# Kernel optimization log

Measured on AMD Instinct MI355X. Metric: run time of the kernel, lower is better.

Reference implementation:

```python
import jax, jax.numpy as jnp
import numpy as np

L = 2          # num_hidden_layers
B, S, H = 2, 2048, 1024
NH, DH = 16, 64   # heads, head dim
FF = 4096
EPS = 1e-5


def setup_inputs() -> dict:
    key = jax.random.key(0)
    ks = jax.random.split(key, 20)
    s = 0.02
    inp = {
        "hidden_states": jax.random.normal(ks[0], (B, S, H), jnp.float32),
        "attention_mask": jnp.zeros((B, 1, 1, S), jnp.float32),
        "Wq": jax.random.normal(ks[1], (L, H, H), jnp.float32) * s,
        "bq": jnp.zeros((L, H), jnp.float32),
        "Wk": jax.random.normal(ks[2], (L, H, H), jnp.float32) * s,
        "bk": jnp.zeros((L, H), jnp.float32),
        "Wv": jax.random.normal(ks[3], (L, H, H), jnp.float32) * s,
        "bv": jnp.zeros((L, H), jnp.float32),
        "Wao": jax.random.normal(ks[4], (L, H, H), jnp.float32) * s,
        "bao": jnp.zeros((L, H), jnp.float32),
        "ln1_g": jnp.ones((L, H), jnp.float32),
        "ln1_b": jnp.zeros((L, H), jnp.float32),
        "Wi": jax.random.normal(ks[5], (L, H, FF), jnp.float32) * s,
        "bi": jnp.zeros((L, FF), jnp.float32),
        "Wo": jax.random.normal(ks[6], (L, FF, H), jnp.float32) * s,
        "bo": jnp.zeros((L, H), jnp.float32),
        "ln2_g": jnp.ones((L, H), jnp.float32),
        "ln2_b": jnp.zeros((L, H), jnp.float32),
    }
    return inp


def _layernorm(x, g, b):
    m = jnp.mean(x, axis=-1, keepdims=True)
    v = jnp.var(x, axis=-1, keepdims=True)
    return (x - m) * jax.lax.rsqrt(v + EPS) * g + b


def _split_heads(x):
    # [B,S,H] -> [B,NH,S,DH]
    return x.reshape(B, S, NH, DH).transpose(0, 2, 1, 3)


def _layer(x, mask, Wq, bq, Wk, bk, Wv, bv, Wao, bao, g1, b1, Wi, bi, Wo, bo, g2, b2):
    q = _split_heads(x @ Wq + bq)
    k = _split_heads(x @ Wk + bk)
    v = _split_heads(x @ Wv + bv)
    scores = jnp.einsum('bhqd,bhkd->bhqk', q, k) / np.sqrt(DH).astype(np.float32)
    scores = scores + mask  # additive attention mask
    probs = jax.nn.softmax(scores, axis=-1)
    ctx = jnp.einsum('bhqk,bhkd->bhqd', probs, v)
    ctx = ctx.transpose(0, 2, 1, 3).reshape(B, S, H)
    x = _layernorm(ctx @ Wao + bao + x, g1, b1)
    ffn = jax.nn.gelu(x @ Wi + bi, approximate=False) @ Wo + bo
    return _layernorm(ffn + x, g2, b2)


def reference(hidden_states, attention_mask, Wq, bq, Wk, bk, Wv, bv, Wao, bao,
              ln1_g, ln1_b, Wi, bi, Wo, bo, ln2_g, ln2_b):
    x = hidden_states
    for i in range(L):
        x = _layer(x, attention_mask,
                   Wq[i], bq[i], Wk[i], bk[i], Wv[i], bv[i], Wao[i], bao[i],
                   ln1_g[i], ln1_b[i], Wi[i], bi[i], Wo[i], bo[i], ln2_g[i], ln2_b[i])
    return x
```

## Files before the change

kernel.cpp:

```cpp
#include <hip/hip_runtime.h>

typedef _Float16 half_t;
typedef _Float16 half8  __attribute__((ext_vector_type(8)));
typedef _Float16 half4v __attribute__((ext_vector_type(4)));
typedef float    f32x4  __attribute__((ext_vector_type(4)));

#define AS1 __attribute__((address_space(1)))
#define AS3 __attribute__((address_space(3)))

#define MODE_H16  0
#define MODE_F32R 1
#define MODE_GELU 2

__device__ __forceinline__ f32x4 zero4() {
    f32x4 z; z[0] = 0.f; z[1] = 0.f; z[2] = 0.f; z[3] = 0.f; return z;
}

__device__ __forceinline__ half8 lds_frag(const half_t* p) {
    union { uint4 u; half8 h; } c;
    c.u = *(const uint4*)p;
    return c.h;
}

__device__ __forceinline__ float gelu_f(float v) {
    float t = v * v;
    float u = v * (1.595769122f + 0.0713548163f * t);
    return v / (1.f + __expf(-u));
}

__device__ __forceinline__ void gl_lds16(const half_t* g, half_t* l) {
    __builtin_amdgcn_global_load_lds(
        (AS1 unsigned int*)(unsigned long long)(const void*)g,
        (AS3 unsigned int*)l,
        16, 0, 0);
}



__device__ __forceinline__ void stage_half(
    const half_t* __restrict__ G, half_t* L, int K, int srow, int sck, int w)
{
    gl_lds16(G + (size_t)srow * K + sck,        L + w * 512);
    gl_lds16(G + (size_t)(64 + srow) * K + sck, L + 4096 + w * 512);
}

#define LDA(MH)                                                              \
    _Pragma("unroll")                                                        \
    for (int m = 0; m < 4; m++) {                                            \
        af[m][0] = lds_frag(&Ad[abase + (MH) * 4096 + m * 1024 + c0]);       \
        af[m][1] = lds_frag(&Ad[abase + (MH) * 4096 + m * 1024 + c1]);       \
    }

#define LDB(NH)                                                              \
    _Pragma("unroll")                                                        \
    for (int n = 0; n < 2; n++) {                                            \
        bf[NH][n][0] = lds_frag(&Bd[bbase + (NH) * 2048 + n * 1024 + c0]);   \
        bf[NH][n][1] = lds_frag(&Bd[bbase + (NH) * 2048 + n * 1024 + c1]);   \
    }

#define MFMA_Q(MH, NH)                                                       \
    _Pragma("unroll")                                                        \
    for (int m = 0; m < 4; m++)                                              \
        _Pragma("unroll")                                                    \
        for (int n = 0; n < 2; n++) {                                        \
            acc[(MH)*4 + m][(NH)*2 + n] =                                    \
                __builtin_amdgcn_mfma_f32_16x16x32_f16(                      \
                    af[m][0], bf[NH][n][0], acc[(MH)*4 + m][(NH)*2 + n],     \
                    0, 0, 0);                                                \
            acc[(MH)*4 + m][(NH)*2 + n] =                                    \
                __builtin_amdgcn_mfma_f32_16x16x32_f16(                      \
                    af[m][1], bf[NH][n][1], acc[(MH)*4 + m][(NH)*2 + n],     \
                    0, 0, 0);                                                \
        }

__device__ __forceinline__ void mfma_core256(
    const half_t* __restrict__ Ag, const half_t* __restrict__ Bg, int K,
    half_t* As, half_t* Bs, f32x4 (&acc)[8][4])
{
    const int tid  = threadIdx.x;
    const int w    = tid >> 6, lane = tid & 63;
    const int wm   = w >> 2, wn = w & 3;
    const int g    = lane >> 4, ml = lane & 15, m7 = ml & 7;
    const int srow = tid >> 3;
    const int sck  = ((tid & 7) ^ (srow & 7)) * 8;

#pragma unroll
    for (int i = 0; i < 8; i++)
#pragma unroll
        for (int j = 0; j < 4; j++) acc[i][j] = zero4();

    const int abase = (wm * 128 + ml) * 64;
    const int bbase = (wn * 64 + ml) * 64;
    const int c0 = (g ^ m7) * 8, c1 = ((4 + g) ^ m7) * 8;

    stage_half(Ag, As, K, srow, sck, w);
    stage_half(Ag + (size_t)128 * K, As + 8192, K, srow, sck, w);
    stage_half(Bg, Bs, K, srow, sck, w);
    stage_half(Bg + (size_t)128 * K, Bs + 8192, K, srow, sck, w);
    asm volatile("s_waitcnt vmcnt(0)" ::: "memory");
    __builtin_amdgcn_s_barrier();

    const int NT = K >> 6;
    half8 af[4][2];
    half8 bf[2][2][2];

    for (int t = 0; t < NT; ++t) {
        half_t* Ad = As + (t & 1) * 16384;
        half_t* Bd = Bs + (t & 1) * 16384;
        half_t* An = As + ((t + 1) & 1) * 16384;
        half_t* Bn = Bs + ((t + 1) & 1) * 16384;
        const half_t* Agn = Ag + (t + 1) * 64;
        const half_t* Bgn = Bg + (t + 1) * 64;
        const bool pf = (t + 1 < NT);

        LDA(0)
        LDB(0)
        if (pf) {
            stage_half(Agn, An, K, srow, sck, w);
            stage_half(Agn + (size_t)128 * K, An + 8192, K, srow, sck, w);
        }
        __builtin_amdgcn_s_barrier();
        __builtin_amdgcn_s_setprio(1);
        MFMA_Q(0, 0)
        __builtin_amdgcn_s_setprio(0);
        __builtin_amdgcn_s_barrier();

        LDB(1)
        if (pf) {
            stage_half(Bgn, Bn, K, srow, sck, w);
            stage_half(Bgn + (size_t)128 * K, Bn + 8192, K, srow, sck, w);
        }
        __builtin_amdgcn_s_barrier();
        __builtin_amdgcn_s_setprio(1);
        MFMA_Q(0, 1)
        __builtin_amdgcn_s_setprio(0);
        __builtin_amdgcn_s_barrier();

        LDA(1)
        __builtin_amdgcn_s_barrier();
        __builtin_amdgcn_s_setprio(1);
        MFMA_Q(1, 1)
        __builtin_amdgcn_s_setprio(0);
        __builtin_amdgcn_s_barrier();

        __builtin_amdgcn_s_setprio(1);
        MFMA_Q(1, 0)
        __builtin_amdgcn_s_setprio(0);
        asm volatile("s_waitcnt vmcnt(0)" ::: "memory");
        __builtin_amdgcn_s_barrier();
    }
}

__global__ __launch_bounds__(512, 2) void gemm256_bt(
    const half_t* __restrict__ A,
    const half_t* __restrict__ Bt,
    const float*  __restrict__ bias,
    const float*  __restrict__ res,
    void* __restrict__ out,
    int M, int N, int K, int mode)
{
    __shared__ __align__(16) half_t As[2 * 16384];
    __shared__ __align__(16) half_t Bs[2 * 16384];

    const int m0 = blockIdx.y * 256, n0 = blockIdx.x * 256;
    f32x4 acc[8][4];
    mfma_core256(A + (size_t)m0 * K, Bt + (size_t)n0 * K, K, As, Bs, acc);

    const int tid = threadIdx.x;
    const int w   = tid >> 6, lane = tid & 63;
    const int wm  = w >> 2, wn = w & 3;
    const int g   = lane >> 4, ml = lane & 15;
    const int gm0 = m0 + wm * 128, gn0 = n0 + wn * 64;

#pragma unroll
    for (int nj = 0; nj < 4; nj++) {
        int col = gn0 + nj * 16 + ml;
        float bv = bias[col];
#pragma unroll
        for (int mi = 0; mi < 8; mi++) {
#pragma unroll
            for (int r = 0; r < 4; r++) {
                int row = gm0 + mi * 16 + g * 4 + r;
                float v = acc[mi][nj][r] + bv;
                size_t idx = (size_t)row * N + col;
                if (mode == MODE_F32R) {
                    ((float*)out)[idx] = v + res[idx];
                } else if (mode == MODE_GELU) {
                    ((half_t*)out)[idx] = (half_t)gelu_f(v);
                } else {
                    ((half_t*)out)[idx] = (half_t)v;
                }
            }
        }
    }
}

__global__ __launch_bounds__(512, 2) void gemm256_qkv(
    const half_t* __restrict__ A,
    const half_t* __restrict__ Bt,
    const float*  __restrict__ bq,
    const float*  __restrict__ bk,
    const float*  __restrict__ bv,
    half_t* __restrict__ Qo, half_t* __restrict__ Ko, half_t* __restrict__ Vto,
    int M, int K)
{
    __shared__ __align__(16) half_t As[2 * 16384];
    __shared__ __align__(16) half_t Bs[2 * 16384];

    const int m0 = blockIdx.y * 256, n0 = blockIdx.x * 256;
    f32x4 acc[8][4];
    mfma_core256(A + (size_t)m0 * K, Bt + (size_t)n0 * K, K, As, Bs, acc);

    const int tid = threadIdx.x;
    const int w   = tid >> 6, lane = tid & 63;
    const int wm  = w >> 2, wn = w & 3;
    const int g   = lane >> 4, ml = lane & 15;

    const int seg   = n0 >> 10;
    const int nbase = (n0 & 1023) + wn * 64;
    const float* bias = (seg == 0) ? bq : (seg == 1) ? bk : bv;
    const int gm0 = m0 + wm * 128;

    if (seg < 2) {
        half_t* O = (seg == 0) ? Qo : Ko;
#pragma unroll
        for (int nj = 0; nj < 4; nj++) {
            int col = nbase + nj * 16 + ml;
            float bvv = bias[col];
#pragma unroll
            for (int mi = 0; mi < 8; mi++)
#pragma unroll
                for (int r = 0; r < 4; r++)
                    O[(size_t)(gm0 + mi * 16 + g * 4 + r) * 1024 + col] =
                        (half_t)(acc[mi][nj][r] + bvv);
        }
    } else {
#pragma unroll
        for (int nj = 0; nj < 4; nj++) {
            int col = nbase + nj * 16 + ml;
            float bvv = bias[col];
#pragma unroll
            for (int mi = 0; mi < 8; mi++) {
                int rowb = gm0 + mi * 16 + g * 4;
                int bb = rowb >> 11, sl = rowb & 2047;
                half4v v4;
#pragma unroll
                for (int r = 0; r < 4; r++) v4[r] = (half_t)(acc[mi][nj][r] + bvv);
                *(half4v*)&Vto[((size_t)bb * 1024 + col) * 2048 + sl] = v4;
            }
        }
    }
}

__global__ __launch_bounds__(256) void gemm_bt64(
    const half_t* __restrict__ A,
    const half_t* __restrict__ Bt,
    const float*  __restrict__ bias,
    const float*  __restrict__ res,
    float* __restrict__ out,
    int M, int N, int K)
{
    __shared__ __align__(16) half_t As[128 * 64];
    __shared__ __align__(16) half_t Bs[64 * 64];

    const int tid  = threadIdx.x;
    const int w    = tid >> 6, lane = tid & 63;
    const int m0   = blockIdx.y * 128, n0 = blockIdx.x * 64;
    const int g    = lane >> 4, ml = lane & 15, m7 = ml & 7;
    const int mo   = w * 32;
    const int r8   = lane >> 3;
    const int sck  = ((lane & 7) ^ (r8 & 7)) * 8;

    f32x4 acc[2][4];
#pragma unroll
    for (int i = 0; i < 2; i++)
#pragma unroll
        for (int j = 0; j < 4; j++) acc[i][j] = zero4();

    const half_t* Ag = A  + (size_t)m0 * K;
    const half_t* Bg = Bt + (size_t)n0 * K;

    for (int k0 = 0; k0 < K; k0 += 64) {
        __syncthreads();
#pragma unroll
        for (int i = 0; i < 4; i++) {
            int t = w * 4 + i;
            gl_lds16(Ag + (size_t)(t * 8 + r8) * K + k0 + sck, &As[t * 512]);
        }
#pragma unroll
        for (int i = 0; i < 2; i++) {
            int t = w * 2 + i;
            gl_lds16(Bg + (size_t)(t * 8 + r8) * K + k0 + sck, &Bs[t * 512]);
        }
        __syncthreads();
#pragma unroll
        for (int kk = 0; kk < 2; kk++) {
            const int co = ((kk * 4 + g) ^ m7) * 8;
            half8 af[2], bf[4];
#pragma unroll
            for (int i = 0; i < 2; i++) af[i] = lds_frag(&As[(mo + i * 16 + ml) * 64 + co]);
#pragma unroll
            for (int j = 0; j < 4; j++) bf[j] = lds_frag(&Bs[(j * 16 + ml) * 64 + co]);
#pragma unroll
            for (int i = 0; i < 2; i++)
#pragma unroll
                for (int j = 0; j < 4; j++)
                    acc[i][j] = __builtin_amdgcn_mfma_f32_16x16x32_f16(af[i], bf[j], acc[i][j], 0, 0, 0);
        }
    }

    const int gm0 = m0 + mo;
#pragma unroll
    for (int j = 0; j < 4; j++) {
        int col = n0 + j * 16 + ml;
        float bv = bias[col];
#pragma unroll
        for (int i = 0; i < 2; i++) {
#pragma unroll
            for (int r = 0; r < 4; r++) {
                int row = gm0 + i * 16 + g * 4 + r;
                size_t idx = (size_t)row * N + col;
                out[idx] = acc[i][j][r] + bv + res[idx];
            }
        }
    }
}

__global__ __launch_bounds__(256, 4) void flash_attn(
    const half_t* __restrict__ Q,
    const half_t* __restrict__ Kq,
    const half_t* __restrict__ Vt,
    const float*  __restrict__ mask,
    half_t* __restrict__ opart,
    float2* __restrict__ mlpart,
    int S, int H)
{
    __shared__ __align__(16) half_t Ks[64 * 64];
    __shared__ __align__(16) half_t Vs[64 * 64];
    __shared__ __align__(16) half_t Ps[4 * 32 * 64];

    const int qt = blockIdx.x, h = blockIdx.y, z = blockIdx.z;
    const int b = z >> 1, hf = z & 1;
    const int tid = threadIdx.x, w = tid >> 6, lane = tid & 63;
    const int g = lane >> 4, ml = lane & 15, m7 = ml & 7;
    const int NHloc = gridDim.y;
    const int BNHS = 2 * NHloc * S;

    const int q0 = qt * 128 + w * 32;
    const half_t* Qg = Q  + ((size_t)(b * S + q0)) * H + h * 64;
    const half_t* Kg = Kq + ((size_t)b * S) * H + h * 64;
    const half_t* Vg = Vt + ((size_t)b * H + h * 64) * (size_t)S;
    const float*  mk = mask + (size_t)b * S;

    half8 qf[2][2];
#pragma unroll
    for (int qi = 0; qi < 2; qi++)
#pragma unroll
        for (int kk = 0; kk < 2; kk++)
            qf[qi][kk] = *(const half8*)(Qg + (size_t)(qi * 16 + ml) * H + kk * 32 + g * 8);

    float m_[2] = {-1e30f, -1e30f}, l_[2] = {0.f, 0.f};
    f32x4 o[2][4];
#pragma unroll
    for (int qi = 0; qi < 2; qi++)
#pragma unroll
        for (int df = 0; df < 4; df++) o[qi][df] = zero4();

    half_t* Pw = &Ps[w * 32 * 64];
    const int srow = tid >> 3;
    const int sc   = tid & 7;

    const int kvbeg = hf * (S >> 1), kvend = kvbeg + (S >> 1);
    for (int kv0 = kvbeg; kv0 < kvend; kv0 += 64) {
        __syncthreads();
#pragma unroll
        for (int t = 0; t < 2; t++) {
            int row = t * 32 + srow;
            int ck  = sc ^ (row & 7);
            gl_lds16(Kg + (size_t)(kv0 + row) * H + ck * 8, &Ks[(t * 256 + w * 64) * 8]);
            gl_lds16(Vg + (size_t)row * S + kv0 + ck * 8,   &Vs[(t * 256 + w * 64) * 8]);
        }
        __syncthreads();

        f32x4 s[2][4];
#pragma unroll
        for (int kvf = 0; kvf < 4; kvf++) {
            half8 k0 = lds_frag(&Ks[(kvf * 16 + ml) * 64 + ((0 + g) ^ m7) * 8]);
            half8 k1 = lds_frag(&Ks[(kvf * 16 + ml) * 64 + ((4 + g) ^ m7) * 8]);
            s[0][kvf] = __builtin_amdgcn_mfma_f32_16x16x32_f16(k0, qf[0][0], zero4(), 0, 0, 0);
            s[0][kvf] = __builtin_amdgcn_mfma_f32_16x16x32_f16(k1, qf[0][1], s[0][kvf], 0, 0, 0);
            s[1][kvf] = __builtin_amdgcn_mfma_f32_16x16x32_f16(k0, qf[1][0], zero4(), 0, 0, 0);
            s[1][kvf] = __builtin_amdgcn_mfma_f32_16x16x32_f16(k1, qf[1][1], s[1][kvf], 0, 0, 0);
        }
#pragma unroll
        for (int kvf = 0; kvf < 4; kvf++) {
            float4 mv = *(const float4*)(mk + kv0 + kvf * 16 + g * 4);
#pragma unroll
            for (int qi = 0; qi < 2; qi++) {
                s[qi][kvf][0] = s[qi][kvf][0] * 0.125f + mv.x;
                s[qi][kvf][1] = s[qi][kvf][1] * 0.125f + mv.y;
                s[qi][kvf][2] = s[qi][kvf][2] * 0.125f + mv.z;
                s[qi][kvf][3] = s[qi][kvf][3] * 0.125f + mv.w;
            }
        }
        float alpha[2];
#pragma unroll
        for (int qi = 0; qi < 2; qi++) {
            float mx = -1e30f;
#pragma unroll
            for (int kvf = 0; kvf < 4; kvf++)
#pragma unroll
                for (int r = 0; r < 4; r++) mx = fmaxf(mx, s[qi][kvf][r]);
            mx = fmaxf(mx, __shfl_xor(mx, 16));
            mx = fmaxf(mx, __shfl_xor(mx, 32));
            float mnew = fmaxf(m_[qi], mx);
            alpha[qi]  = __expf(m_[qi] - mnew);
            m_[qi] = mnew;
            float ps = 0.f;
#pragma unroll
            for (int kvf = 0; kvf < 4; kvf++)
#pragma unroll
                for (int r = 0; r < 4; r++) {
                    float pv = __expf(s[qi][kvf][r] - mnew);
                    s[qi][kvf][r] = pv; ps += pv;
                }
            ps += __shfl_xor(ps, 16);
            ps += __shfl_xor(ps, 32);
            l_[qi] = l_[qi] * alpha[qi] + ps;
#pragma unroll
            for (int kvf = 0; kvf < 4; kvf++) {
                half4v pk;
#pragma unroll
                for (int r = 0; r < 4; r++) pk[r] = (half_t)s[qi][kvf][r];
                *(half4v*)(Pw + (qi * 16 + ml) * 64 +
                           (((kvf * 2 + (g >> 1)) ^ m7) * 8) + (g & 1) * 4) = pk;
            }
        }
#pragma unroll
        for (int qi = 0; qi < 2; qi++) {
#pragma unroll
            for (int r = 0; r < 4; r++) {
                float a = __shfl(alpha[qi], (lane & 48) + g * 4 + r);
#pragma unroll
                for (int df = 0; df < 4; df++) o[qi][df][r] *= a;
            }
        }
#pragma unroll
        for (int kk = 0; kk < 2; kk++) {
            half8 pa0 = lds_frag(&Pw[(ml)      * 64 + ((kk * 4 + g) ^ m7) * 8]);
            half8 pa1 = lds_frag(&Pw[(16 + ml) * 64 + ((kk * 4 + g) ^ m7) * 8]);
#pragma unroll
            for (int df = 0; df < 4; df++) {
                half8 vb = lds_frag(&Vs[(df * 16 + ml) * 64 + ((kk * 4 + g) ^ m7) * 8]);
                o[0][df] = __builtin_amdgcn_mfma_f32_16x16x32_f16(pa0, vb, o[0][df], 0, 0, 0);
                o[1][df] = __builtin_amdgcn_mfma_f32_16x16x32_f16(pa1, vb, o[1][df], 0, 0, 0);
            }
        }
    }

    const size_t rowbase = (size_t)hf * BNHS + ((size_t)(b * NHloc + h)) * S + q0;
#pragma unroll
    for (int qi = 0; qi < 2; qi++) {
#pragma unroll
        for (int r = 0; r < 4; r++) {
            size_t ro = (rowbase + qi * 16 + g * 4 + r) * 64;
#pragma unroll
            for (int df = 0; df < 4; df++)
                opart[ro + df * 16 + ml] = (half_t)o[qi][df][r];
        }
    }
    if (g == 0) {
#pragma unroll
        for (int qi = 0; qi < 2; qi++)
            mlpart[rowbase + qi * 16 + ml] = make_float2(m_[qi], l_[qi]);
    }
}

__global__ __launch_bounds__(256) void flash_merge(
    const half_t* __restrict__ opart,
    const float2* __restrict__ mlpart,
    half_t* __restrict__ ctx)
{
    int gid = blockIdx.x * 256 + threadIdx.x;
    int row = gid >> 4, dg = (gid & 15) * 4;
    float2 a = mlpart[row], c = mlpart[65536 + row];
    float m  = fmaxf(a.x, c.x);
    float w1 = __expf(a.x - m), w2 = __expf(c.x - m);
    float inv = 1.f / (w1 * a.y + w2 * c.y);
    half4v o1 = *(const half4v*)&opart[(size_t)row * 64 + dg];
    half4v o2 = *(const half4v*)&opart[(size_t)(65536 + row) * 64 + dg];
    int b = row >> 15, hq = row & 32767;
    int h = hq >> 11, q = hq & 2047;
    half4v o;
#pragma unroll
    for (int i = 0; i < 4; i++)
        o[i] = (half_t)((w1 * (float)o1[i] + w2 * (float)o2[i]) * inv);
    *(half4v*)&ctx[((size_t)(b * 2048 + q)) * 1024 + h * 64 + dg] = o;
}

__global__ __launch_bounds__(256) void transpose_cast(
    const float* __restrict__ W, half_t* __restrict__ Wt, int Kd, int Nd)
{
    __shared__ float tile[32][33];
    size_t zoff = (size_t)blockIdx.z * Kd * Nd;
    const float* Wz = W + zoff;
    half_t* Wtz = Wt + zoff;
    int n0 = blockIdx.x * 32, k0 = blockIdx.y * 32;
    int tx = threadIdx.x & 31, ty = threadIdx.x >> 5;
#pragma unroll
    for (int j = 0; j < 4; j++)
        tile[ty + j * 8][tx] = Wz[(size_t)(k0 + ty + j * 8) * Nd + n0 + tx];
    __syncthreads();
#pragma unroll
    for (int j = 0; j < 4; j++)
        Wtz[(size_t)(n0 + ty + j * 8) * Kd + k0 + tx] = (half_t)tile[tx][ty + j * 8];
}

__global__ __launch_bounds__(256) void transpose_qkv(
    const float* __restrict__ Wq, const float* __restrict__ Wk,
    const float* __restrict__ Wv, half_t* __restrict__ WT)
{
    __shared__ float tile[32][33];
    int z = blockIdx.z, l = z / 3, which = z % 3;
    const float* W = ((which == 0) ? Wq : (which == 1) ? Wk : Wv) + (size_t)l * 1024 * 1024;
    half_t* D = WT + ((size_t)l * 3 + which) * 1024 * 1024;
    int n0 = blockIdx.x * 32, k0 = blockIdx.y * 32;
    int tx = threadIdx.x & 31, ty = threadIdx.x >> 5;
#pragma unroll
    for (int j = 0; j < 4; j++)
        tile[ty + j * 8][tx] = W[(size_t)(k0 + ty + j * 8) * 1024 + n0 + tx];
    __syncthreads();
#pragma unroll
    for (int j = 0; j < 4; j++)
        D[(size_t)(n0 + ty + j * 8) * 1024 + k0 + tx] = (half_t)tile[tx][ty + j * 8];
}

__global__ __launch_bounds__(256) void cast_f32_f16(
    const float* __restrict__ in, half_t* __restrict__ out)
{
    int i = blockIdx.x * 256 + threadIdx.x;
    float4 v = ((const float4*)in)[i];
    half4v o; o[0] = (half_t)v.x; o[1] = (half_t)v.y; o[2] = (half_t)v.z; o[3] = (half_t)v.w;
    *(half4v*)(out + (size_t)i * 4) = o;
}

__global__ __launch_bounds__(256) void layernorm_k(
    const float* __restrict__ in,
    const float* __restrict__ gam, const float* __restrict__ bet,
    float* __restrict__ outf, half_t* __restrict__ outh)
{
    int row = blockIdx.x, tid = threadIdx.x;
    const float4 v = ((const float4*)(in + (size_t)row * 1024))[tid];
    float s = v.x + v.y + v.z + v.w;
    float q = v.x * v.x + v.y * v.y + v.z * v.z + v.w * v.w;
    for (int off = 32; off; off >>= 1) { s += __shfl_down(s, off); q += __shfl_down(q, off); }
    __shared__ float ss[4], sq[4];
    int w = tid >> 6;
    if ((tid & 63) == 0) { ss[w] = s; sq[w] = q; }
    __syncthreads();
    float S_ = ss[0] + ss[1] + ss[2] + ss[3];
    float Q_ = sq[0] + sq[1] + sq[2] + sq[3];
    float mean = S_ * (1.f / 1024.f);
    float var  = Q_ * (1.f / 1024.f) - mean * mean;
    float rstd = rsqrtf(var + 1e-5f);
    float4 gm = ((const float4*)gam)[tid];
    float4 bt = ((const float4*)bet)[tid];
    float y0 = (v.x - mean) * rstd * gm.x + bt.x;
    float y1 = (v.y - mean) * rstd * gm.y + bt.y;
    float y2 = (v.z - mean) * rstd * gm.z + bt.z;
    float y3 = (v.w - mean) * rstd * gm.w + bt.w;
    ((float4*)(outf + (size_t)row * 1024))[tid] = make_float4(y0, y1, y2, y3);
    half4v oh; oh[0] = (half_t)y0; oh[1] = (half_t)y1; oh[2] = (half_t)y2; oh[3] = (half_t)y3;
    *(half4v*)(outh + (size_t)row * 1024 + tid * 4) = oh;
}

extern "C" void kernel_launch(void* const* d_in, const int* in_sizes, int n_in,
                              void* d_out, int out_size, void* d_ws, size_t ws_size,
                              hipStream_t stream)
{
    const int Lc = 2, Bb = 2, S = 2048, Hh = 1024, NH = 16, FF = 4096;
    const int M = Bb * S;

    const float* hs   = (const float*)d_in[0];
    const float* mask = (const float*)d_in[1];
    const float* Wq   = (const float*)d_in[2];  const float* bq  = (const float*)d_in[3];
    const float* Wk   = (const float*)d_in[4];  const float* bk  = (const float*)d_in[5];
    const float* Wv   = (const float*)d_in[6];  const float* bv  = (const float*)d_in[7];
    const float* Wao  = (const float*)d_in[8];  const float* bao = (const float*)d_in[9];
    const float* g1   = (const float*)d_in[10]; const float* b1  = (const float*)d_in[11];
    const float* Wi   = (const float*)d_in[12]; const float* bi  = (const float*)d_in[13];
    const float* Wo   = (const float*)d_in[14]; const float* bo  = (const float*)d_in[15];
    const float* g2   = (const float*)d_in[16]; const float* b2  = (const float*)d_in[17];

    char* p = (char*)d_ws;
    auto take = [&](size_t bytes) { char* r = p; p += (bytes + 255) & ~(size_t)255; return r; };

    half_t* WqkvT = (half_t*)take((size_t)Lc * 3 * Hh * Hh * 2);
    half_t* WaoT  = (half_t*)take((size_t)Lc * Hh * Hh * 2);
    half_t* WiT   = (half_t*)take((size_t)Lc * Hh * FF * 2);
    half_t* WoT   = (half_t*)take((size_t)Lc * FF * Hh * 2);
    half_t* xb    = (half_t*)take((size_t)M * Hh * 2);
    half_t* Qb    = (half_t*)take((size_t)M * Hh * 2);
    half_t* Kb2   = (half_t*)take((size_t)M * Hh * 2);
    half_t* Vtb   = (half_t*)take((size_t)M * Hh * 2);
    (void)          take((size_t)M * Hh * 2);
    half_t* h1    = Qb;
    float*  t0    = (float*)take((size_t)M * Hh * 4);
    float*  x1f   = (float*)take((size_t)M * Hh * 4);
    half_t* x1b   = (half_t*)take((size_t)M * Hh * 2);

    half_t* opart  = (half_t*)t0;
    float2* mlpart = (float2*)x1b;

    dim3 tb(256);

    transpose_qkv<<<dim3(32, 32, Lc * 3), tb, 0, stream>>>(Wq, Wk, Wv, WqkvT);
    transpose_cast<<<dim3(32, 32, Lc), tb, 0, stream>>>(Wao, WaoT, Hh, Hh);
    transpose_cast<<<dim3(FF / 32, 32, Lc), tb, 0, stream>>>(Wi, WiT, Hh, FF);
    transpose_cast<<<dim3(32, FF / 32, Lc), tb, 0, stream>>>(Wo, WoT, FF, Hh);
    cast_f32_f16<<<dim3(M * Hh / 1024), tb, 0, stream>>>(hs, xb);

    const float* xres = hs;
    for (int l = 0; l < Lc; l++) {
        const half_t* WqkvTl = WqkvT + (size_t)l * 3 * Hh * Hh;
        const half_t* WaoTl  = WaoT  + (size_t)l * Hh * Hh;
        const half_t* WiTl   = WiT   + (size_t)l * Hh * FF;
        const half_t* WoTl   = WoT   + (size_t)l * FF * Hh;

        gemm256_qkv<<<dim3(3072 / 256, M / 256), dim3(512), 0, stream>>>(
            xb, WqkvTl, bq + l * Hh, bk + l * Hh, bv + l * Hh, Qb, Kb2, Vtb, M, Hh);

        flash_attn<<<dim3(S / 128, NH, Bb * 2), tb, 0, stream>>>(
            Qb, Kb2, Vtb, mask, opart, mlpart, S, Hh);
        flash_merge<<<dim3(Bb * NH * S * 16 / 256), tb, 0, stream>>>(opart, mlpart, xb);

        gemm_bt64<<<dim3(Hh / 64, M / 128), tb, 0, stream>>>(
            xb, WaoTl, bao + l * Hh, xres, t0, M, Hh, Hh);
        layernorm_k<<<dim3(M), tb, 0, stream>>>(t0, g1 + l * Hh, b1 + l * Hh, x1f, x1b);

        gemm256_bt<<<dim3(FF / 256, M / 256), dim3(512), 0, stream>>>(
            x1b, WiTl, bi + l * FF, nullptr, h1, M, FF, Hh, MODE_GELU);
        gemm_bt64<<<dim3(Hh / 64, M / 128), tb, 0, stream>>>(
            h1, WoTl, bo + l * Hh, x1f, t0, M, Hh, FF);

        float* outf = (l == Lc - 1) ? (float*)d_out : x1f;
        layernorm_k<<<dim3(M), tb, 0, stream>>>(t0, g2 + l * Hh, b2 + l * Hh, outf, xb);
        xres = x1f;
    }
}
```

Baseline: 683.4 us.

## Split-K the FFN down GEMM, double-buffer flash KV, use exp2 with lazy rescale

The FFN output GEMM moves from a 64-wide tile kernel to the 256x256 MFMA core with a 4-way split-K. Partial sums go to a new fp32 workspace, and a new layernorm kernel reduces them along with the bias and residual, so more of the grid fills the GPU at the cost of extra partial-sum memory traffic. Flash attention now double-buffers the K/V LDS tiles to overlap loads with compute and drops one barrier per iteration. It also switches to exp2 with pre-scaled log2e, skips rescaling the output when the running max barely changes, and lowers occupancy to 3 blocks to fit the extra LDS.

```diff
diff --git a/kernel.cpp b/kernel.cpp
--- a/kernel.cpp
+++ b/kernel.cpp
@@ -26,6 +26,10 @@
     float t = v * v;
     float u = v * (1.595769122f + 0.0713548163f * t);
     return v / (1.f + __expf(-u));
+}
+
+__device__ __forceinline__ float fexp2(float x) {
+    return __builtin_amdgcn_exp2f(x);
 }
 
 __device__ __forceinline__ void gl_lds16(const half_t* g, half_t* l) {
@@ -74,7 +78,8 @@
         }
 
 __device__ __forceinline__ void mfma_core256(
-    const half_t* __restrict__ Ag, const half_t* __restrict__ Bg, int K,
+    const half_t* __restrict__ Ag, const half_t* __restrict__ Bg,
+    int K, int KT,
     half_t* As, half_t* Bs, f32x4 (&acc)[8][4])
 {
     const int tid  = threadIdx.x;
@@ -100,18 +105,17 @@
     asm volatile("s_waitcnt vmcnt(0)" ::: "memory");
     __builtin_amdgcn_s_barrier();
 
-    const int NT = K >> 6;
     half8 af[4][2];
     half8 bf[2][2][2];
 
-    for (int t = 0; t < NT; ++t) {
+    for (int t = 0; t < KT; ++t) {
         half_t* Ad = As + (t & 1) * 16384;
         half_t* Bd = Bs + (t & 1) * 16384;
         half_t* An = As + ((t + 1) & 1) * 16384;
         half_t* Bn = Bs + ((t + 1) & 1) * 16384;
         const half_t* Agn = Ag + (t + 1) * 64;
         const half_t* Bgn = Bg + (t + 1) * 64;
-        const bool pf = (t + 1 < NT);
+        const bool pf = (t + 1 < KT);
 
         LDA(0)
         LDB(0)
@@ -164,7 +168,7 @@
 
     const int m0 = blockIdx.y * 256, n0 = blockIdx.x * 256;
     f32x4 acc[8][4];
-    mfma_core256(A + (size_t)m0 * K, Bt + (size_t)n0 * K, K, As, Bs, acc);
+    mfma_core256(A + (size_t)m0 * K, Bt + (size_t)n0 * K, K, K >> 6, As, Bs, acc);
 
     const int tid = threadIdx.x;
     const int w   = tid >> 6, lane = tid & 63;
@@ -195,6 +199,43 @@
     }
 }
 
+__global__ __launch_bounds__(512, 2) void gemm256_sk(
+    const half_t* __restrict__ A,
+    const half_t* __restrict__ Bt,
+    float* __restrict__ part,
+    int M, int N, int K, int KS)
+{
+    __shared__ __align__(16) half_t As[2 * 16384];
+    __shared__ __align__(16) half_t Bs[2 * 16384];
+
+    const int m0 = blockIdx.y * 256, n0 = blockIdx.x * 256;
+    const int sk = blockIdx.z;
+    f32x4 acc[8][4];
+    mfma_core256(A + (size_t)m0 * K + (size_t)sk * KS,
+                 Bt + (size_t)n0 * K + (size_t)sk * KS,
+                 K, KS >> 6, As, Bs, acc);
+
+    const int tid = threadIdx.x;
+    const int w   = tid >> 6, lane = tid & 63;
+    const int wm  = w >> 2, wn = w & 3;
+    const int g   = lane >> 4, ml = lane & 15;
+    const int gm0 = m0 + wm * 128, gn0 = n0 + wn * 64;
+    float* P = part + (size_t)sk * M * N;
+
+#pragma unroll
+    for (int nj = 0; nj < 4; nj++) {
+        int col = gn0 + nj * 16 + ml;
+#pragma unroll
+        for (int mi = 0; mi < 8; mi++) {
+#pragma unroll
+            for (int r = 0; r < 4; r++) {
+                int row = gm0 + mi * 16 + g * 4 + r;
+                P[(size_t)row * N + col] = acc[mi][nj][r];
+            }
+        }
+    }
+}
+
 __global__ __launch_bounds__(512, 2) void gemm256_qkv(
     const half_t* __restrict__ A,
     const half_t* __restrict__ Bt,
@@ -209,7 +250,7 @@
 
     const int m0 = blockIdx.y * 256, n0 = blockIdx.x * 256;
     f32x4 acc[8][4];
-    mfma_core256(A + (size_t)m0 * K, Bt + (size_t)n0 * K, K, As, Bs, acc);
+    mfma_core256(A + (size_t)m0 * K, Bt + (size_t)n0 * K, K, K >> 6, As, Bs, acc);
 
     const int tid = threadIdx.x;
     const int w   = tid >> 6, lane = tid & 63;
@@ -326,7 +367,7 @@
     }
 }
 
-__global__ __launch_bounds__(256, 4) void flash_attn(
+__global__ __launch_bounds__(256, 3) void flash_attn(
     const half_t* __restrict__ Q,
     const half_t* __restrict__ Kq,
     const half_t* __restrict__ Vt,
@@ -335,9 +376,12 @@
     float2* __restrict__ mlpart,
     int S, int H)
 {
-    __shared__ __align__(16) half_t Ks[64 * 64];
-    __shared__ __align__(16) half_t Vs[64 * 64];
+    __shared__ __align__(16) half_t Ks[2][64 * 64];
+    __shared__ __align__(16) half_t Vs[2][64 * 64];
     __shared__ __align__(16) half_t Ps[4 * 32 * 64];
+
+    const float LOG2E = 1.44269504f;
+    const float SCL2  = 0.125f * 1.44269504f;
 
     const int qt = blockIdx.x, h = blockIdx.y, z = blockIdx.z;
     const int b = z >> 1, hf = z & 1;
@@ -370,40 +414,54 @@
     const int srow = tid >> 3;
     const int sc   = tid & 7;
 
-    const int kvbeg = hf * (S >> 1), kvend = kvbeg + (S >> 1);
-    for (int kv0 = kvbeg; kv0 < kvend; kv0 += 64) {
-        __syncthreads();
+    auto stage_kv = [&](int buf, int kv0) {
 #pragma unroll
         for (int t = 0; t < 2; t++) {
             int row = t * 32 + srow;
             int ck  = sc ^ (row & 7);
-            gl_lds16(Kg + (size_t)(kv0 + row) * H + ck * 8, &Ks[(t * 256 + w * 64) * 8]);
-            gl_lds16(Vg + (size_t)row * S + kv0 + ck * 8,   &Vs[(t * 256 + w * 64) * 8]);
-        }
-        __syncthreads();
+            gl_lds16(Kg + (size_t)(kv0 + row) * H + ck * 8, &Ks[buf][t * 2048 + w * 512]);
+            gl_lds16(Vg + (size_t)row * S + kv0 + ck * 8,   &Vs[buf][t * 2048 + w * 512]);
+        }
+    };
+
+    const int kvbeg = hf * (S >> 1), kvend = kvbeg + (S >> 1);
+
+    stage_kv(0, kvbeg);
+    __syncthreads();
+
+    int bufc = 0;
+    for (int kv0 = kvbeg; kv0 < kvend; kv0 += 64) {
+        if (kv0 + 64 < kvend) stage_kv(bufc ^ 1, kv0 + 64);
 
         f32x4 s[2][4];
+        __builtin_amdgcn_s_setprio(1);
 #pragma unroll
         for (int kvf = 0; kvf < 4; kvf++) {
-            half8 k0 = lds_frag(&Ks[(kvf * 16 + ml) * 64 + ((0 + g) ^ m7) * 8]);
-            half8 k1 = lds_frag(&Ks[(kvf * 16 + ml) * 64 + ((4 + g) ^ m7) * 8]);
+            half8 k0 = lds_frag(&Ks[bufc][(kvf * 16 + ml) * 64 + ((0 + g) ^ m7) * 8]);
+            half8 k1 = lds_frag(&Ks[bufc][(kvf * 16 + ml) * 64 + ((4 + g) ^ m7) * 8]);
             s[0][kvf] = __builtin_amdgcn_mfma_f32_16x16x32_f16(k0, qf[0][0], zero4(), 0, 0, 0);
             s[0][kvf] = __builtin_amdgcn_mfma_f32_16x16x32_f16(k1, qf[0][1], s[0][kvf], 0, 0, 0);
             s[1][kvf] = __builtin_amdgcn_mfma_f32_16x16x32_f16(k0, qf[1][0], zero4(), 0, 0, 0);
             s[1][kvf] = __builtin_amdgcn_mfma_f32_16x16x32_f16(k1, qf[1][1], s[1][kvf], 0, 0, 0);
         }
+        __builtin_amdgcn_s_setprio(0);
+
 #pragma unroll
         for (int kvf = 0; kvf < 4; kvf++) {
             float4 mv = *(const float4*)(mk + kv0 + kvf * 16 + g * 4);
+            float mv0 = mv.x * LOG2E, mv1 = mv.y * LOG2E;
+            float mv2 = mv.z * LOG2E, mv3 = mv.w * LOG2E;
 #pragma unroll
             for (int qi = 0; qi < 2; qi++) {
-                s[qi][kvf][0] = s[qi][kvf][0] * 0.125f + mv.x;
-                s[qi][kvf][1] = s[qi][kvf][1] * 0.125f + mv.y;
-                s[qi][kvf][2] = s[qi][kvf][2] * 0.125f + mv.z;
-                s[qi][kvf][3] = s[qi][kvf][3] * 0.125f + mv.w;
+                s[qi][kvf][0] = s[qi][kvf][0] * SCL2 + mv0;
+                s[qi][kvf][1] = s[qi][kvf][1] * SCL2 + mv1;
+                s[qi][kvf][2] = s[qi][kvf][2] * SCL2 + mv2;
+                s[qi][kvf][3] = s[qi][kvf][3] * SCL2 + mv3;
             }
         }
+
         float alpha[2];
+        bool  defer[2];
 #pragma unroll
         for (int qi = 0; qi < 2; qi++) {
             float mx = -1e30f;
@@ -413,20 +471,23 @@
                 for (int r = 0; r < 4; r++) mx = fmaxf(mx, s[qi][kvf][r]);
             mx = fmaxf(mx, __shfl_xor(mx, 16));
             mx = fmaxf(mx, __shfl_xor(mx, 32));
-            float mnew = fmaxf(m_[qi], mx);
-            alpha[qi]  = __expf(m_[qi] - mnew);
+            defer[qi] = __all(mx <= m_[qi] + 11.5f);
+            float mnew, al;
+            if (defer[qi]) { mnew = m_[qi]; al = 1.f; }
+            else           { mnew = fmaxf(m_[qi], mx); al = fexp2(m_[qi] - mnew); }
+            alpha[qi] = al;
             m_[qi] = mnew;
             float ps = 0.f;
 #pragma unroll
             for (int kvf = 0; kvf < 4; kvf++)
 #pragma unroll
                 for (int r = 0; r < 4; r++) {
-                    float pv = __expf(s[qi][kvf][r] - mnew);
+                    float pv = fexp2(s[qi][kvf][r] - mnew);
                     s[qi][kvf][r] = pv; ps += pv;
                 }
             ps += __shfl_xor(ps, 16);
             ps += __shfl_xor(ps, 32);
-            l_[qi] = l_[qi] * alpha[qi] + ps;
+            l_[qi] = l_[qi] * al + ps;
 #pragma unroll
             for (int kvf = 0; kvf < 4; kvf++) {
                 half4v pk;
@@ -438,24 +499,32 @@
         }
 #pragma unroll
         for (int qi = 0; qi < 2; qi++) {
-#pragma unroll
-            for (int r = 0; r < 4; r++) {
-                float a = __shfl(alpha[qi], (lane & 48) + g * 4 + r);
-#pragma unroll
-                for (int df = 0; df < 4; df++) o[qi][df][r] *= a;
+            if (!defer[qi]) {
+#pragma unroll
+                for (int r = 0; r < 4; r++) {
+                    float a = __shfl(alpha[qi], (lane & 48) + g * 4 + r);
+#pragma unroll
+                    for (int df = 0; df < 4; df++) o[qi][df][r] *= a;
+                }
             }
         }
+
+        __builtin_amdgcn_s_setprio(1);
 #pragma unroll
         for (int kk = 0; kk < 2; kk++) {
             half8 pa0 = lds_frag(&Pw[(ml)      * 64 + ((kk * 4 + g) ^ m7) * 8]);
             half8 pa1 = lds_frag(&Pw[(16 + ml) * 64 + ((kk * 4 + g) ^ m7) * 8]);
 #pragma unroll
             for (int df = 0; df < 4; df++) {
-                half8 vb = lds_frag(&Vs[(df * 16 + ml) * 64 + ((kk * 4 + g) ^ m7) * 8]);
+                half8 vb = lds_frag(&Vs[bufc][(df * 16 + ml) * 64 + ((kk * 4 + g) ^ m7) * 8]);
                 o[0][df] = __builtin_amdgcn_mfma_f32_16x16x32_f16(pa0, vb, o[0][df], 0, 0, 0);
                 o[1][df] = __builtin_amdgcn_mfma_f32_16x16x32_f16(pa1, vb, o[1][df], 0, 0, 0);
             }
         }
+        __builtin_amdgcn_s_setprio(0);
+
+        __syncthreads();
+        bufc ^= 1;
     }
 
     const size_t rowbase = (size_t)hf * BNHS + ((size_t)(b * NHloc + h)) * S + q0;
@@ -485,7 +554,7 @@
     int row = gid >> 4, dg = (gid & 15) * 4;
     float2 a = mlpart[row], c = mlpart[65536 + row];
     float m  = fmaxf(a.x, c.x);
-    float w1 = __expf(a.x - m), w2 = __expf(c.x - m);
+    float w1 = fexp2(a.x - m), w2 = fexp2(c.x - m);
     float inv = 1.f / (w1 * a.y + w2 * c.y);
     half4v o1 = *(const half4v*)&opart[(size_t)row * 64 + dg];
     half4v o2 = *(const half4v*)&opart[(size_t)(65536 + row) * 64 + dg];
@@ -574,6 +643,50 @@
     *(half4v*)(outh + (size_t)row * 1024 + tid * 4) = oh;
 }
 
+__global__ __launch_bounds__(256) void layernorm_sk(
+    const float* __restrict__ part,
+    const float* __restrict__ bias,
+    const float* __restrict__ res,
+    const float* __restrict__ gam, const float* __restrict__ bet,
+    float* __restrict__ outf, half_t* __restrict__ outh)
+{
+    const size_t SP = (size_t)4096 * 1024;
+    int row = blockIdx.x, tid = threadIdx.x;
+    size_t o = (size_t)row * 1024 + tid * 4;
+    float4 v0 = *(const float4*)(part + o);
+    float4 v1 = *(const float4*)(part + SP + o);
+    float4 v2 = *(const float4*)(part + 2 * SP + o);
+    float4 v3 = *(const float4*)(part + 3 * SP + o);
+    float4 rv = *(const float4*)(res + o);
+    float4 bb = ((const float4*)bias)[tid];
+    float x0 = v0.x + v1.x + v2.x + v3.x + bb.x + rv.x;
+    float x1 = v0.y + v1.y + v2.y + v3.y + bb.y + rv.y;
+    float x2 = v0.z + v1.z + v2.z + v3.z + bb.z + rv.z;
+    float x3 = v0.w + v1.w + v2.w + v3.w + bb.w + rv.w;
+
+    float s = x0 + x1 + x2 + x3;
+    float q = x0 * x0 + x1 * x1 + x2 * x2 + x3 * x3;
+    for (int off = 32; off; off >>= 1) { s += __shfl_down(s, off); q += __shfl_down(q, off); }
+    __shared__ float ss[4], sq[4];
+    int w = tid >> 6;
+    if ((tid & 63) == 0) { ss[w] = s; sq[w] = q; }
+    __syncthreads();
+    float S_ = ss[0] + ss[1] + ss[2] + ss[3];
+    float Q_ = sq[0] + sq[1] + sq[2] + sq[3];
+    float mean = S_ * (1.f / 1024.f);
+    float var  = Q_ * (1.f / 1024.f) - mean * mean;
+    float rstd = rsqrtf(var + 1e-5f);
+    float4 gm = ((const float4*)gam)[tid];
+    float4 bt = ((const float4*)bet)[tid];
+    float y0 = (x0 - mean) * rstd * gm.x + bt.x;
+    float y1 = (x1 - mean) * rstd * gm.y + bt.y;
+    float y2 = (x2 - mean) * rstd * gm.z + bt.z;
+    float y3 = (x3 - mean) * rstd * gm.w + bt.w;
+    ((float4*)(outf + (size_t)row * 1024))[tid] = make_float4(y0, y1, y2, y3);
+    half4v oh; oh[0] = (half_t)y0; oh[1] = (half_t)y1; oh[2] = (half_t)y2; oh[3] = (half_t)y3;
+    *(half4v*)(outh + (size_t)row * 1024 + tid * 4) = oh;
+}
+
 extern "C" void kernel_launch(void* const* d_in, const int* in_sizes, int n_in,
                               void* d_out, int out_size, void* d_ws, size_t ws_size,
                               hipStream_t stream)
@@ -608,6 +721,7 @@
     float*  t0    = (float*)take((size_t)M * Hh * 4);
     float*  x1f   = (float*)take((size_t)M * Hh * 4);
     half_t* x1b   = (half_t*)take((size_t)M * Hh * 2);
+    float*  part  = (float*)take((size_t)4 * M * Hh * 4);
 
     half_t* opart  = (half_t*)t0;
     float2* mlpart = (float2*)x1b;
@@ -640,11 +754,13 @@
 
         gemm256_bt<<<dim3(FF / 256, M / 256), dim3(512), 0, stream>>>(
             x1b, WiTl, bi + l * FF, nullptr, h1, M, FF, Hh, MODE_GELU);
-        gemm_bt64<<<dim3(Hh / 64, M / 128), tb, 0, stream>>>(
-            h1, WoTl, bo + l * Hh, x1f, t0, M, Hh, FF);
+
+        gemm256_sk<<<dim3(Hh / 256, M / 256, 4), dim3(512), 0, stream>>>(
+            h1, WoTl, part, M, Hh, FF, FF / 4);
 
         float* outf = (l == Lc - 1) ? (float*)d_out : x1f;
-        layernorm_k<<<dim3(M), tb, 0, stream>>>(t0, g2 + l * Hh, b2 + l * Hh, outf, xb);
+        layernorm_sk<<<dim3(M), tb, 0, stream>>>(
+            part, bo + l * Hh, x1f, g2 + l * Hh, b2 + l * Hh, outf, xb);
         xres = x1f;
     }
 }
```

After: 710.2 us. 3.9% more time.
